# Optimization experiments

Measured on AMD Instinct MI355X. Metric: run time of the kernel, lower is better.

Reference implementation:

```python
import jax, jax.numpy as jnp
import numpy as np

# The torch code implements pixel shifts via bmm with sparse permutation
# matrices: T[i,i+1]=1. bmm(x, T) moves column j-1 -> j (shift right, zero col 0);
# bmm(x, T^T) shifts left; bmm(T, x) moves row j+1 -> j (shift up, zero last row);
# bmm(T^T, x) shifts down. We implement these directly as pad+slice gathers.

def _shift_right(x):  # [B,H,W]
    return jnp.pad(x[:, :, :-1], ((0, 0), (0, 0), (1, 0)))

def _shift_left(x):
    return jnp.pad(x[:, :, 1:], ((0, 0), (0, 0), (0, 1)))

def _shift_up(x):
    return jnp.pad(x[:, 1:, :], ((0, 0), (0, 1), (0, 0)))

def _shift_down(x):
    return jnp.pad(x[:, :-1, :], ((0, 0), (1, 0), (0, 0)))

def _bce_sum(p, t):
    # torch.nn.BCELoss(reduction='sum') clamps log terms at -100
    logp = jnp.clip(jnp.log(p), -100.0, None)
    log1mp = jnp.clip(jnp.log1p(-p), -100.0, None)
    return -jnp.sum(t * logp + (1.0 - t) * log1mp)

def setup_inputs() -> dict:
    key = jax.random.key(0)
    k1, k2, k3 = jax.random.split(key, 3)
    B, C, H, W = 16, 8, 512, 512
    c_map = jax.random.normal(k1, (B, C, H, W), dtype=jnp.float32)
    target = jax.random.bernoulli(k2, 0.5, (B, 1, H, W)).astype(jnp.float32)
    con_target = jax.random.bernoulli(k3, 0.5, (B, C, H, W)).astype(jnp.float32)
    return {"c_map": c_map, "target": target, "con_target": con_target}

def reference(c_map, target, con_target):
    p = jax.nn.sigmoid(c_map)  # [B,8,H,W]

    sum_conn = jnp.sum(con_target, axis=1)  # [B,H,W]
    edge = ((sum_conn < 8.0) & (sum_conn > 0.0)).astype(p.dtype)

    c0, c1, c2, c3 = p[:, 0], p[:, 1], p[:, 2], p[:, 3]
    c4, c5, c6, c7 = p[:, 4], p[:, 5], p[:, 6], p[:, 7]

    right = _shift_right(c4)
    left = _shift_left(c3)
    left_bottom = _shift_left(_shift_down(c5))
    right_above = _shift_right(_shift_up(c2))
    left_above = _shift_left(_shift_up(c0))
    bottom = _shift_down(c6)
    up = _shift_up(c1)
    right_bottom = _shift_right(_shift_down(c7))

    a1 = c3 * right
    a2 = c4 * left
    a3 = c1 * bottom
    a4 = c6 * up
    a5 = c2 * left_bottom
    a6 = c5 * right_above
    a7 = c0 * right_bottom
    a8 = c7 * left_above

    vote_out = jnp.stack([a7, a3, a5, a1, a2, a6, a4, a8], axis=1)  # [B,8,H,W]

    glo_map = jnp.mean(vote_out, axis=1)       # [B,H,W]
    pred_mask_min = jnp.min(vote_out, axis=1)  # [B,H,W]
    decouple_map = glo_map * (1.0 - edge) + (1.0 - pred_mask_min) * edge

    de_loss = _bce_sum(decouple_map[:, None], target)
    conmap_l = _bce_sum(p, con_target)
    bimap_l = _bce_sum(vote_out, con_target)
    return 0.8 * conmap_l + de_loss + 0.2 * bimap_l
```

## Files before the change

kernel.cpp:

```cpp
#include <hip/hip_runtime.h>
#include <math.h>

#define NB 16
#define NC 8
#define HH 512
#define WW 512
#define HW (HH * WW)
#define CHW (NC * HW)

__device__ __forceinline__ float sigf(float x) {
    return __fdividef(1.0f, 1.0f + __expf(-x));
}

__device__ __forceinline__ float bce_term(float t, float p) {
    float q = (t > 0.5f) ? p : (1.0f - p);
    return -fmaxf(__logf(q), -100.0f);
}

__device__ __forceinline__ void ld4(const float* p, float* o) {
    float4 v = *(const float4*)p;
    o[0] = v.x; o[1] = v.y; o[2] = v.z; o[3] = v.w;
}

__global__ __launch_bounds__(256)
__attribute__((amdgpu_waves_per_eu(2, 4)))
void bicon_loss_kernel(
    const float* __restrict__ c_map,
    const float* __restrict__ target,
    const float* __restrict__ con_target,
    float* __restrict__ out)
{
    const int tid = blockIdx.x * 256 + threadIdx.x;
    const int w0 = (tid & 127) << 2;
    const int h  = (tid >> 7) & (HH - 1);
    const int b  = tid >> 16;

    const float* cm = c_map      + b * CHW + h * WW + w0;
    const float* ct = con_target + b * CHW + h * WW + w0;

    const bool hu = (h > 0), hd = (h < HH - 1);
    const bool wl = (w0 > 0), wr = (w0 + 4 < WW);
    const int ru = hu ? -WW : 0;
    const int rd = hd ?  WW : 0;

    float cv[8][4];
    #pragma unroll
    for (int c = 0; c < 8; ++c) ld4(cm + c * HW, cv[c]);

    float u6r[4], u5r[4], u7r[4];
    ld4(cm + 6 * HW + ru, u6r);
    ld4(cm + 5 * HW + ru, u5r);
    ld4(cm + 7 * HW + ru, u7r);

    float d1r[4], d2r[4], d0r[4];
    ld4(cm + 1 * HW + rd, d1r);
    ld4(cm + 2 * HW + rd, d2r);
    ld4(cm + 0 * HW + rd, d0r);

    float tv[8][4];
    #pragma unroll
    for (int c = 0; c < 8; ++c) ld4(ct + c * HW, tv[c]);

    float tg[4];
    ld4(target + b * HW + h * WW + w0, tg);

    const float u5e = cm[5 * HW + ru + (wr ? 4 : 0)];
    const float u7e = cm[7 * HW + ru + (wl ? -1 : 0)];
    const float d2e = cm[2 * HW + rd + (wr ? 4 : 0)];
    const float d0e = cm[0 * HW + rd + (wl ? -1 : 0)];
    const float m4e = cm[4 * HW + (wl ? -1 : 0)];
    const float m3e = cm[3 * HW + (wr ? 4 : 0)];

    float sp[8][4];
    #pragma unroll
    for (int c = 0; c < 8; ++c)
        #pragma unroll
        for (int j = 0; j < 4; ++j) sp[c][j] = sigf(cv[c][j]);

    float acc_con = 0.0f, acc_bi = 0.0f, acc_de = 0.0f;
    #pragma unroll
    for (int j = 0; j < 4; ++j) {
        const float n6 = hu ? sigf(u6r[j]) : 0.0f;
        const float n5 = (j < 3) ? (hu ? sigf(u5r[j + 1]) : 0.0f)
                                 : ((hu && wr) ? sigf(u5e) : 0.0f);
        const float n7 = (j > 0) ? (hu ? sigf(u7r[j - 1]) : 0.0f)
                                 : ((hu && wl) ? sigf(u7e) : 0.0f);
        const float dn1 = hd ? sigf(d1r[j]) : 0.0f;
        const float dn2 = (j < 3) ? (hd ? sigf(d2r[j + 1]) : 0.0f)
                                  : ((hd && wr) ? sigf(d2e) : 0.0f);
        const float dn0 = (j > 0) ? (hd ? sigf(d0r[j - 1]) : 0.0f)
                                  : ((hd && wl) ? sigf(d0e) : 0.0f);
        const float m4 = (j > 0) ? sp[4][j - 1] : (wl ? sigf(m4e) : 0.0f);
        const float m3 = (j < 3) ? sp[3][j + 1] : (wr ? sigf(m3e) : 0.0f);

        const float a1 = sp[3][j] * m4;
        const float a2 = sp[4][j] * m3;
        const float a3 = sp[1][j] * n6;
        const float a4 = sp[6][j] * dn1;
        const float a5 = sp[2][j] * n5;
        const float a6 = sp[5][j] * dn2;
        const float a7 = sp[0][j] * n7;
        const float a8 = sp[7][j] * dn0;

        const float vote[8] = { a7, a3, a5, a1, a2, a6, a4, a8 };

        float sum_conn = 0.0f;
        #pragma unroll
        for (int c = 0; c < 8; ++c) sum_conn += tv[c][j];

        #pragma unroll
        for (int c = 0; c < 8; ++c) {
            acc_con += bce_term(tv[c][j], sp[c][j]);
            acc_bi  += bce_term(tv[c][j], vote[c]);
        }

        const float glo = (a1 + a2 + a3 + a4 + a5 + a6 + a7 + a8) * 0.125f;
        float mn = vote[0];
        #pragma unroll
        for (int c = 1; c < 8; ++c) mn = fminf(mn, vote[c]);

        const bool edge = (sum_conn < 8.0f) && (sum_conn > 0.0f);
        const float dec = edge ? (1.0f - mn) : glo;
        acc_de += bce_term(tg[j], dec);
    }

    float local = fmaf(0.8f, acc_con, fmaf(0.2f, acc_bi, acc_de));

    #pragma unroll
    for (int off = 32; off > 0; off >>= 1)
        local += __shfl_down(local, off, 64);

    __shared__ float wsum[4];
    const int lane = threadIdx.x & 63;
    const int wid  = threadIdx.x >> 6;
    if (lane == 0) wsum[wid] = local;
    __syncthreads();
    if (threadIdx.x == 0) {
        atomicAdd(out, wsum[0] + wsum[1] + wsum[2] + wsum[3]);
    }
}

extern "C" void kernel_launch(void* const* d_in, const int* in_sizes, int n_in,
                              void* d_out, int out_size, void* d_ws, size_t ws_size,
                              hipStream_t stream) {
    const float* c_map      = (const float*)d_in[0];
    const float* target     = (const float*)d_in[1];
    const float* con_target = (const float*)d_in[2];
    float* out = (float*)d_out;

    hipMemsetAsync(out, 0, sizeof(float), stream);

    const int total_threads = NB * HH * (WW / 4);
    const int blocks = total_threads / 256;
    bicon_loss_kernel<<<blocks, 256, 0, stream>>>(c_map, target, con_target, out);
}
```

Measured before the change: 293.0 us.

## Stage c_map rows with halos into LDS via direct global-to-LDS loads

Each block now handles two image rows and loads the needed c_map planes (center rows plus up and down halo rows) into shared memory with global_load_lds, then reads neighbours from LDS. This replaces the repeated per-thread global loads of halo rows and scalar edge elements. It also drops the waves_per_eu hint. The large LDS footprint per block may reduce occupancy, and the added barrier serializes the load and compute phases.

```diff
diff --git a/kernel.cpp b/kernel.cpp
--- a/kernel.cpp
+++ b/kernel.cpp
@@ -7,6 +7,9 @@
 #define WW 512
 #define HW (HH * WW)
 #define CHW (NC * HW)
+
+typedef const __attribute__((address_space(1))) void* gvp;
+typedef __attribute__((address_space(3))) void*       lvp;
 
 __device__ __forceinline__ float sigf(float x) {
     return __fdividef(1.0f, 1.0f + __expf(-x));
@@ -22,76 +25,90 @@
     o[0] = v.x; o[1] = v.y; o[2] = v.z; o[3] = v.w;
 }
 
-__global__ __launch_bounds__(256)
-__attribute__((amdgpu_waves_per_eu(2, 4)))
-void bicon_loss_kernel(
+__global__ __launch_bounds__(256) void bicon_loss_kernel(
     const float* __restrict__ c_map,
     const float* __restrict__ target,
     const float* __restrict__ con_target,
     float* __restrict__ out)
 {
-    const int tid = blockIdx.x * 256 + threadIdx.x;
-    const int w0 = (tid & 127) << 2;
-    const int h  = (tid >> 7) & (HH - 1);
-    const int b  = tid >> 16;
+    __shared__ float lds[22][WW];
 
-    const float* cm = c_map      + b * CHW + h * WW + w0;
-    const float* ct = con_target + b * CHW + h * WW + w0;
+    const int b    = blockIdx.x >> 8;
+    const int h0   = (blockIdx.x & 255) << 1;
+    const int tid  = threadIdx.x;
+    const int wave = tid >> 6;
+    const int lane = tid & 63;
 
-    const bool hu = (h > 0), hd = (h < HH - 1);
-    const bool wl = (w0 > 0), wr = (w0 + 4 < WW);
-    const int ru = hu ? -WW : 0;
-    const int rd = hd ?  WW : 0;
+    for (int s = wave; s < 44; s += 4) {
+        const int plane = s >> 1, half = s & 1;
+        int ch, rel;
+        if      (plane < 3)  { ch = 5 + plane;  rel = -1; }
+        else if (plane < 11) { ch = plane - 3;  rel = 0;  }
+        else if (plane < 19) { ch = plane - 11; rel = 1;  }
+        else                 { ch = plane - 19; rel = 2;  }
+        int rr = h0 + rel;
+        rr = rr < 0 ? 0 : (rr > HH - 1 ? HH - 1 : rr);
+        const float* gp = c_map + b * CHW + ch * HW + rr * WW + half * 256 + lane * 4;
+        __builtin_amdgcn_global_load_lds((gvp)gp, (lvp)&lds[plane][half * 256], 16, 0, 0);
+    }
 
-    float cv[8][4];
-    #pragma unroll
-    for (int c = 0; c < 8; ++c) ld4(cm + c * HW, cv[c]);
+    const int r   = tid >> 7;
+    const int px0 = (tid & 127) << 2;
+    const int gr  = h0 + r;
 
-    float u6r[4], u5r[4], u7r[4];
-    ld4(cm + 6 * HW + ru, u6r);
-    ld4(cm + 5 * HW + ru, u5r);
-    ld4(cm + 7 * HW + ru, u7r);
-
-    float d1r[4], d2r[4], d0r[4];
-    ld4(cm + 1 * HW + rd, d1r);
-    ld4(cm + 2 * HW + rd, d2r);
-    ld4(cm + 0 * HW + rd, d0r);
-
+    const float* ct = con_target + b * CHW + gr * WW + px0;
     float tv[8][4];
     #pragma unroll
     for (int c = 0; c < 8; ++c) ld4(ct + c * HW, tv[c]);
+    float tg[4];
+    ld4(target + b * HW + gr * WW + px0, tg);
 
-    float tg[4];
-    ld4(target + b * HW + h * WW + w0, tg);
+    __syncthreads();
 
-    const float u5e = cm[5 * HW + ru + (wr ? 4 : 0)];
-    const float u7e = cm[7 * HW + ru + (wl ? -1 : 0)];
-    const float d2e = cm[2 * HW + rd + (wr ? 4 : 0)];
-    const float d0e = cm[0 * HW + rd + (wl ? -1 : 0)];
-    const float m4e = cm[4 * HW + (wl ? -1 : 0)];
-    const float m3e = cm[3 * HW + (wr ? 4 : 0)];
+    const bool hu = gr > 0, hd = gr < HH - 1;
+    const bool wl = px0 > 0, wr = px0 < WW - 4;
+
+    const int cb = r ? 11 : 3;
+    const int pu5 = r ? 8 : 0, pu6 = r ? 9 : 1, pu7 = r ? 10 : 2;
+    const int pd0 = r ? 19 : 11, pd1 = r ? 20 : 12, pd2 = r ? 21 : 13;
 
     float sp[8][4];
     #pragma unroll
-    for (int c = 0; c < 8; ++c)
+    for (int c = 0; c < 8; ++c) {
+        float cv[4]; ld4(&lds[cb + c][px0], cv);
         #pragma unroll
-        for (int j = 0; j < 4; ++j) sp[c][j] = sigf(cv[c][j]);
+        for (int j = 0; j < 4; ++j) sp[c][j] = sigf(cv[j]);
+    }
+
+    float u5[4], u6[4], u7[4], dd0[4], dd1[4], dd2[4];
+    ld4(&lds[pu5][px0], u5);
+    ld4(&lds[pu6][px0], u6);
+    ld4(&lds[pu7][px0], u7);
+    ld4(&lds[pd0][px0], dd0);
+    ld4(&lds[pd1][px0], dd1);
+    ld4(&lds[pd2][px0], dd2);
+    const float e5  = lds[pu5][wr ? px0 + 4 : px0];
+    const float e7  = lds[pu7][wl ? px0 - 1 : px0];
+    const float e2  = lds[pd2][wr ? px0 + 4 : px0];
+    const float e0  = lds[pd0][wl ? px0 - 1 : px0];
+    const float m4e = lds[cb + 4][wl ? px0 - 1 : px0];
+    const float m3e = lds[cb + 3][wr ? px0 + 4 : px0];
 
     float acc_con = 0.0f, acc_bi = 0.0f, acc_de = 0.0f;
     #pragma unroll
     for (int j = 0; j < 4; ++j) {
-        const float n6 = hu ? sigf(u6r[j]) : 0.0f;
-        const float n5 = (j < 3) ? (hu ? sigf(u5r[j + 1]) : 0.0f)
-                                 : ((hu && wr) ? sigf(u5e) : 0.0f);
-        const float n7 = (j > 0) ? (hu ? sigf(u7r[j - 1]) : 0.0f)
-                                 : ((hu && wl) ? sigf(u7e) : 0.0f);
-        const float dn1 = hd ? sigf(d1r[j]) : 0.0f;
-        const float dn2 = (j < 3) ? (hd ? sigf(d2r[j + 1]) : 0.0f)
-                                  : ((hd && wr) ? sigf(d2e) : 0.0f);
-        const float dn0 = (j > 0) ? (hd ? sigf(d0r[j - 1]) : 0.0f)
-                                  : ((hd && wl) ? sigf(d0e) : 0.0f);
-        const float m4 = (j > 0) ? sp[4][j - 1] : (wl ? sigf(m4e) : 0.0f);
-        const float m3 = (j < 3) ? sp[3][j + 1] : (wr ? sigf(m3e) : 0.0f);
+        const float n6  = hu ? sigf(u6[j]) : 0.0f;
+        const float n5  = (j < 3) ? (hu ? sigf(u5[j + 1]) : 0.0f)
+                                  : ((hu && wr) ? sigf(e5) : 0.0f);
+        const float n7  = (j > 0) ? (hu ? sigf(u7[j - 1]) : 0.0f)
+                                  : ((hu && wl) ? sigf(e7) : 0.0f);
+        const float dn1 = hd ? sigf(dd1[j]) : 0.0f;
+        const float dn2 = (j < 3) ? (hd ? sigf(dd2[j + 1]) : 0.0f)
+                                  : ((hd && wr) ? sigf(e2) : 0.0f);
+        const float dn0 = (j > 0) ? (hd ? sigf(dd0[j - 1]) : 0.0f)
+                                  : ((hd && wl) ? sigf(e0) : 0.0f);
+        const float m4  = (j > 0) ? sp[4][j - 1] : (wl ? sigf(m4e) : 0.0f);
+        const float m3  = (j < 3) ? sp[3][j + 1] : (wr ? sigf(m3e) : 0.0f);
 
         const float a1 = sp[3][j] * m4;
         const float a2 = sp[4][j] * m3;
@@ -131,11 +148,9 @@
         local += __shfl_down(local, off, 64);
 
     __shared__ float wsum[4];
-    const int lane = threadIdx.x & 63;
-    const int wid  = threadIdx.x >> 6;
-    if (lane == 0) wsum[wid] = local;
+    if (lane == 0) wsum[wave] = local;
     __syncthreads();
-    if (threadIdx.x == 0) {
+    if (tid == 0) {
         atomicAdd(out, wsum[0] + wsum[1] + wsum[2] + wsum[3]);
     }
 }
@@ -150,7 +165,6 @@
 
     hipMemsetAsync(out, 0, sizeof(float), stream);
 
-    const int total_threads = NB * HH * (WW / 4);
-    const int blocks = total_threads / 256;
+    const int blocks = NB * (HH / 2);
     bicon_loss_kernel<<<blocks, 256, 0, stream>>>(c_map, target, con_target, out);
 }
```

Result: no change. 291.7 us (-0.4%).
